# Optimization experiments

Hardware: AMD Instinct MI355X
Metric: run time of the kernel (lower is better)

Reference implementation:

```python
import jax, jax.numpy as jnp
import numpy as np

ENT_N = 100000  # entity vocab (relation rows live inside this table, as in the source)
REL_N = 237
DIM = 128
N = 16384       # batch of triples
EPS = 1e-12     # F.normalize default eps


def _l2norm(x, axis=-1):
    n = jnp.linalg.norm(x, axis=axis, keepdims=True)
    return x / jnp.maximum(n, EPS)


def setup_inputs() -> dict:
    key = jax.random.key(0)
    k1, k2, k3, k4 = jax.random.split(key, 4)
    ent_emb = jax.random.normal(k1, (ENT_N, DIM), dtype=jnp.float32)
    h_ids = jax.random.randint(k2, (N,), 0, ENT_N)
    r_typ = jax.random.randint(k3, (N,), 0, REL_N)
    t_ids = jax.random.randint(k4, (N,), 0, ENT_N)
    return {"ent_emb": ent_emb, "h_ids": h_ids, "r_typ": r_typ, "t_ids": t_ids}


def reference(ent_emb, h_ids, r_typ, t_ids):
    d = ent_emb.shape[1]
    h = _l2norm(ent_emb[h_ids])           # [n, d]
    t = _l2norm(ent_emb[t_ids])           # [n, d]
    # The torch loop looks up ent_emb[r_typ*d + k] for k in range(d); gather
    # the whole relation block at once instead of d tiny lookups + cat.
    r_idx = r_typ[:, None] * d + jnp.arange(d)  # [n, d]
    R = ent_emb[r_idx]                     # [n, d, d]; row k = relation vec k
    prod = jnp.einsum('nd,nkd->nk', h, R)  # [n, d]
    prod = _l2norm(prod)
    return jnp.linalg.norm(prod - t, axis=1)  # [n]
```

## Files before the change

### kernel.cpp

```cpp
#include <hip/hip_runtime.h>

#define RELS 237
#define DIM 128
#define CH 32
#define MAXCHUNK 742
#define EPS 1e-12f

typedef __attribute__((ext_vector_type(8))) short bf16x8;
typedef __attribute__((ext_vector_type(4))) float f32x4;


__device__ __forceinline__ unsigned short f2bf(float f) {
    unsigned int u = __float_as_uint(f);
    u = (u + 0x7fffu + ((u >> 16) & 1u)) >> 16;
    return (unsigned short)u;
}

__global__ void k_count(const int* __restrict__ r_typ, int* __restrict__ ws, int n) {
    int i = blockIdx.x * blockDim.x + threadIdx.x;
    if (i < n) atomicAdd(&ws[r_typ[i]], 1);
}

__global__ void k_scanlist(int* __restrict__ ws) {
    __shared__ int scn[256];
    const int t = threadIdx.x;
    const int c = (t < RELS) ? ws[t] : 0;
    scn[t] = c; __syncthreads();
    #pragma unroll
    for (int off = 1; off < 256; off <<= 1) {
        int v = (t >= off) ? scn[t - off] : 0;
        __syncthreads();
        scn[t] += v; __syncthreads();
    }
    const int base = scn[t] - c;
    if (t < RELS) { ws[320 + t] = base; ws[576 + t] = base; }
    const int nch = (c + CH - 1) >> 5;
    __syncthreads();
    scn[t] = nch; __syncthreads();
    #pragma unroll
    for (int off = 1; off < 256; off <<= 1) {
        int v = (t >= off) ? scn[t - off] : 0;
        __syncthreads();
        scn[t] += v; __syncthreads();
    }
    const int choff = scn[t] - nch;
    if (t == 255) ws[300] = scn[255];
    for (int j = 0; j < nch; ++j) {
        int cb  = base + j * CH;
        int len = c - j * CH; if (len > CH) len = CH;
        ws[1024 + choff + j] = (t << 20) | (cb << 6) | len;
    }
}

__global__ void k_scatter(const int* __restrict__ r_typ, int* __restrict__ ws, int n) {
    int i = blockIdx.x * blockDim.x + threadIdx.x;
    if (i < n) {
        int pos = atomicAdd(&ws[576 + r_typ[i]], 1);
        ws[2048 + pos] = i;
    }
}

__global__ __launch_bounds__(256, 3) void relgemm(
    const float* __restrict__ ent,
    const int*   __restrict__ h_ids,
    const int*   __restrict__ t_ids,
    const int*   __restrict__ ws,
    float*       __restrict__ out)
{
    __shared__ char smem[43648];
    unsigned short* Rb = (unsigned short*)smem;
    unsigned short* Hb = (unsigned short*)(smem + 34816);
    int*  sidx = (int*)(smem + 43520);
    float* Pp  = (float*)smem;

    const int cid = blockIdx.x;
    if (cid >= ws[300]) return;
    const int e    = ws[1024 + cid];
    const int r    = e >> 20;
    const int base = (e >> 6) & 16383;
    const int len  = e & 63;
    const int* sorted = ws + 2048;

    const int tid  = threadIdx.x;
    const int lane = tid & 63;
    const int w    = tid >> 6;

    if (tid < CH) {
        int tc = tid < len ? tid : len - 1;
        sidx[tid] = sorted[base + tc];
    }
    __syncthreads();

    const float4* Rg = (const float4*)ent + ((long)r << 12);
    #pragma unroll
    for (int s = 0; s < 16; ++s) {
        int g = s * 256 + tid;
        int row = g >> 5, c4 = g & 31;
        float4 v = Rg[g];
        ushort4 b; b.x = f2bf(v.x); b.y = f2bf(v.y); b.z = f2bf(v.z); b.w = f2bf(v.w);
        *(ushort4*)(Rb + row * 136 + c4 * 4) = b;
    }
    #pragma unroll
    for (int s = 0; s < 4; ++s) {
        int g = s * 256 + tid;
        int trow = g >> 5, c4 = g & 31;
        int hid = h_ids[sidx[trow]];
        float4 v = ((const float4*)ent)[((long)hid << 5) + c4];
        ushort4 b; b.x = f2bf(v.x); b.y = f2bf(v.y); b.z = f2bf(v.z); b.w = f2bf(v.w);
        *(ushort4*)(Hb + trow * 136 + c4 * 4) = b;
    }
    __syncthreads();

    const int q = lane >> 4, c = lane & 15;
    const unsigned short* A0p = Hb + c * 136 + q * 8;
    const unsigned short* A1p = Hb + (c + 16) * 136 + q * 8;
    const unsigned short* B0p = Rb + (w * 32 + c) * 136 + q * 8;
    const unsigned short* B1p = Rb + (w * 32 + 16 + c) * 136 + q * 8;

    f32x4 a00 = {0.f,0.f,0.f,0.f}, a01 = a00, a10 = a00, a11 = a00;
    #pragma unroll
    for (int ks = 0; ks < 4; ++ks) {
        bf16x8 A0 = *(const bf16x8*)(A0p + ks * 32);
        bf16x8 A1 = *(const bf16x8*)(A1p + ks * 32);
        bf16x8 B0 = *(const bf16x8*)(B0p + ks * 32);
        bf16x8 B1 = *(const bf16x8*)(B1p + ks * 32);
        a00 = __builtin_amdgcn_mfma_f32_16x16x32_bf16(A0, B0, a00, 0, 0, 0);
        a01 = __builtin_amdgcn_mfma_f32_16x16x32_bf16(A0, B1, a01, 0, 0, 0);
        a10 = __builtin_amdgcn_mfma_f32_16x16x32_bf16(A1, B0, a10, 0, 0, 0);
        a11 = __builtin_amdgcn_mfma_f32_16x16x32_bf16(A1, B1, a11, 0, 0, 0);
    }
    __syncthreads();

    #pragma unroll
    for (int reg = 0; reg < 4; ++reg) {
        int m0 = q * 4 + reg;
        Pp[m0 * 132        + w * 32      + c] = a00[reg];
        Pp[m0 * 132        + w * 32 + 16 + c] = a01[reg];
        Pp[(m0 + 16) * 132 + w * 32      + c] = a10[reg];
        Pp[(m0 + 16) * 132 + w * 32 + 16 + c] = a11[reg];
    }
    __syncthreads();

    #pragma unroll
    for (int tt = 0; tt < 8; ++tt) {
        int t   = w * 8 + tt;
        int idx = sidx[t];
        int trow = __builtin_amdgcn_readfirstlane(t_ids[idx]);
        const float* tv = ent + ((long)trow << 7);
        float tv0 = tv[lane], tv1 = tv[lane + 64];
        float p0 = Pp[t * 132 + lane], p1 = Pp[t * 132 + 64 + lane];
        float sp  = p0 * p0 + p1 * p1;
        float st  = tv0 * tv0 + tv1 * tv1;
        float spt = p0 * tv0 + p1 * tv1;
        #pragma unroll
        for (int m = 32; m >= 1; m >>= 1) {
            sp  += __shfl_xor(sp,  m, 64);
            st  += __shfl_xor(st,  m, 64);
            spt += __shfl_xor(spt, m, 64);
        }
        if (lane == 0 && t < len) {
            float npn = fmaxf(sqrtf(sp), EPS);
            float ntn = fmaxf(sqrtf(st), EPS);
            float v   = 2.0f - 2.0f * (spt / (npn * ntn));
            out[idx] = sqrtf(fmaxf(v, 0.0f));
        }
    }
}

extern "C" void kernel_launch(void* const* d_in, const int* in_sizes, int n_in,
                              void* d_out, int out_size, void* d_ws, size_t ws_size,
                              hipStream_t stream) {
    const float* ent   = (const float*)d_in[0];
    const int*   h_ids = (const int*)d_in[1];
    const int*   r_typ = (const int*)d_in[2];
    const int*   t_ids = (const int*)d_in[3];
    float* out = (float*)d_out;
    int*   ws  = (int*)d_ws;
    const int n = in_sizes[1];
    const int nb = (n + 255) / 256;

    hipMemsetAsync(ws, 0, 1024, stream);
    hipLaunchKernelGGL(k_count,    dim3(nb),       dim3(256), 0, stream, r_typ, ws, n);
    hipLaunchKernelGGL(k_scanlist, dim3(1),        dim3(256), 0, stream, ws);
    hipLaunchKernelGGL(k_scatter,  dim3(nb),       dim3(256), 0, stream, r_typ, ws, n);
    hipLaunchKernelGGL(relgemm,    dim3(MAXCHUNK), dim3(256), 0, stream,
                       ent, h_ids, t_ids, ws, out);
}
```

Baseline: 122.9 us.

## Double triple-chunk size per relation block and fuse count with scan

Raises the chunk of triples per block from 32 to 64, so each block's load and bf16 conversion of the 128x128 relation matrix is shared by twice as many triples, and each wave now computes four M-tiles. It also folds the count and scan kernels into one, using a last-block-done atomic counter, which removes one launch. The chunk length is stored as len-1 so a length of 64 fits in the 6-bit field. The costs are more LDS per block, fewer blocks in flight, and more padded waste for relations with few triples.

```diff
diff --git a/kernel.cpp b/kernel.cpp
--- a/kernel.cpp
+++ b/kernel.cpp
@@ -2,8 +2,8 @@
 
 #define RELS 237
 #define DIM 128
-#define CH 32
-#define MAXCHUNK 742
+#define CH 64
+#define MAXCHUNK 489
 #define EPS 1e-12f
 
 typedef __attribute__((ext_vector_type(8))) short bf16x8;
@@ -16,15 +16,18 @@
     return (unsigned short)u;
 }
 
-__global__ void k_count(const int* __restrict__ r_typ, int* __restrict__ ws, int n) {
-    int i = blockIdx.x * blockDim.x + threadIdx.x;
+__global__ void k_count_scan(const int* __restrict__ r_typ, int* __restrict__ ws, int n) {
+    __shared__ int scn[256];
+    __shared__ int amLast;
+    const int t = threadIdx.x;
+    const int i = blockIdx.x * blockDim.x + t;
     if (i < n) atomicAdd(&ws[r_typ[i]], 1);
-}
+    __threadfence();
+    if (t == 0) amLast = (atomicAdd(&ws[255], 1) == (int)gridDim.x - 1);
+    __syncthreads();
+    if (!amLast) return;
 
-__global__ void k_scanlist(int* __restrict__ ws) {
-    __shared__ int scn[256];
-    const int t = threadIdx.x;
-    const int c = (t < RELS) ? ws[t] : 0;
+    const int c = (t < RELS) ? atomicAdd(&ws[t], 0) : 0;
     scn[t] = c; __syncthreads();
     #pragma unroll
     for (int off = 1; off < 256; off <<= 1) {
@@ -34,7 +37,7 @@
     }
     const int base = scn[t] - c;
     if (t < RELS) { ws[320 + t] = base; ws[576 + t] = base; }
-    const int nch = (c + CH - 1) >> 5;
+    const int nch = (c + CH - 1) >> 6;
     __syncthreads();
     scn[t] = nch; __syncthreads();
     #pragma unroll
@@ -48,7 +51,7 @@
     for (int j = 0; j < nch; ++j) {
         int cb  = base + j * CH;
         int len = c - j * CH; if (len > CH) len = CH;
-        ws[1024 + choff + j] = (t << 20) | (cb << 6) | len;
+        ws[1024 + choff + j] = (t << 20) | (cb << 6) | (len - 1);
     }
 }
 
@@ -67,10 +70,10 @@
     const int*   __restrict__ ws,
     float*       __restrict__ out)
 {
-    __shared__ char smem[43648];
+    __shared__ char smem[52480];
     unsigned short* Rb = (unsigned short*)smem;
     unsigned short* Hb = (unsigned short*)(smem + 34816);
-    int*  sidx = (int*)(smem + 43520);
+    int*  sidx = (int*)(smem + 52224);
     float* Pp  = (float*)smem;
 
     const int cid = blockIdx.x;
@@ -78,7 +81,7 @@
     const int e    = ws[1024 + cid];
     const int r    = e >> 20;
     const int base = (e >> 6) & 16383;
-    const int len  = e & 63;
+    const int len  = (e & 63) + 1;
     const int* sorted = ws + 2048;
 
     const int tid  = threadIdx.x;
@@ -101,7 +104,7 @@
         *(ushort4*)(Rb + row * 136 + c4 * 4) = b;
     }
     #pragma unroll
-    for (int s = 0; s < 4; ++s) {
+    for (int s = 0; s < 8; ++s) {
         int g = s * 256 + tid;
         int trow = g >> 5, c4 = g & 31;
         int hid = h_ids[sidx[trow]];
@@ -111,39 +114,44 @@
     }
     __syncthreads();
 
-    const int q = lane >> 4, c = lane & 15;
-    const unsigned short* A0p = Hb + c * 136 + q * 8;
-    const unsigned short* A1p = Hb + (c + 16) * 136 + q * 8;
-    const unsigned short* B0p = Rb + (w * 32 + c) * 136 + q * 8;
-    const unsigned short* B1p = Rb + (w * 32 + 16 + c) * 136 + q * 8;
+    const int q = lane >> 4, cc = lane & 15;
+    const unsigned short* Ap0 = Hb + cc * 136 + q * 8;
+    const unsigned short* Bp0 = Rb + (w * 32 + cc) * 136 + q * 8;
+    const unsigned short* Bp1 = Rb + (w * 32 + 16 + cc) * 136 + q * 8;
 
-    f32x4 a00 = {0.f,0.f,0.f,0.f}, a01 = a00, a10 = a00, a11 = a00;
+    f32x4 acc[4][2];
+    #pragma unroll
+    for (int mt = 0; mt < 4; ++mt)
+        #pragma unroll
+        for (int nt = 0; nt < 2; ++nt)
+            acc[mt][nt] = (f32x4){0.f, 0.f, 0.f, 0.f};
+
     #pragma unroll
     for (int ks = 0; ks < 4; ++ks) {
-        bf16x8 A0 = *(const bf16x8*)(A0p + ks * 32);
-        bf16x8 A1 = *(const bf16x8*)(A1p + ks * 32);
-        bf16x8 B0 = *(const bf16x8*)(B0p + ks * 32);
-        bf16x8 B1 = *(const bf16x8*)(B1p + ks * 32);
-        a00 = __builtin_amdgcn_mfma_f32_16x16x32_bf16(A0, B0, a00, 0, 0, 0);
-        a01 = __builtin_amdgcn_mfma_f32_16x16x32_bf16(A0, B1, a01, 0, 0, 0);
-        a10 = __builtin_amdgcn_mfma_f32_16x16x32_bf16(A1, B0, a10, 0, 0, 0);
-        a11 = __builtin_amdgcn_mfma_f32_16x16x32_bf16(A1, B1, a11, 0, 0, 0);
+        bf16x8 B0 = *(const bf16x8*)(Bp0 + ks * 32);
+        bf16x8 B1 = *(const bf16x8*)(Bp1 + ks * 32);
+        #pragma unroll
+        for (int mt = 0; mt < 4; ++mt) {
+            bf16x8 A = *(const bf16x8*)(Ap0 + mt * 16 * 136 + ks * 32);
+            acc[mt][0] = __builtin_amdgcn_mfma_f32_16x16x32_bf16(A, B0, acc[mt][0], 0, 0, 0);
+            acc[mt][1] = __builtin_amdgcn_mfma_f32_16x16x32_bf16(A, B1, acc[mt][1], 0, 0, 0);
+        }
     }
     __syncthreads();
 
     #pragma unroll
-    for (int reg = 0; reg < 4; ++reg) {
-        int m0 = q * 4 + reg;
-        Pp[m0 * 132        + w * 32      + c] = a00[reg];
-        Pp[m0 * 132        + w * 32 + 16 + c] = a01[reg];
-        Pp[(m0 + 16) * 132 + w * 32      + c] = a10[reg];
-        Pp[(m0 + 16) * 132 + w * 32 + 16 + c] = a11[reg];
-    }
+    for (int mt = 0; mt < 4; ++mt)
+        #pragma unroll
+        for (int reg = 0; reg < 4; ++reg) {
+            int m0 = mt * 16 + q * 4 + reg;
+            Pp[m0 * 132 + w * 32      + cc] = acc[mt][0][reg];
+            Pp[m0 * 132 + w * 32 + 16 + cc] = acc[mt][1][reg];
+        }
     __syncthreads();
 
     #pragma unroll
-    for (int tt = 0; tt < 8; ++tt) {
-        int t   = w * 8 + tt;
+    for (int tt = 0; tt < 16; ++tt) {
+        int t   = w * 16 + tt;
         int idx = sidx[t];
         int trow = __builtin_amdgcn_readfirstlane(t_ids[idx]);
         const float* tv = ent + ((long)trow << 7);
@@ -180,9 +188,8 @@
     const int nb = (n + 255) / 256;
 
     hipMemsetAsync(ws, 0, 1024, stream);
-    hipLaunchKernelGGL(k_count,    dim3(nb),       dim3(256), 0, stream, r_typ, ws, n);
-    hipLaunchKernelGGL(k_scanlist, dim3(1),        dim3(256), 0, stream, ws);
-    hipLaunchKernelGGL(k_scatter,  dim3(nb),       dim3(256), 0, stream, r_typ, ws, n);
-    hipLaunchKernelGGL(relgemm,    dim3(MAXCHUNK), dim3(256), 0, stream,
+    hipLaunchKernelGGL(k_count_scan, dim3(nb),       dim3(256), 0, stream, r_typ, ws, n);
+    hipLaunchKernelGGL(k_scatter,    dim3(nb),       dim3(256), 0, stream, r_typ, ws, n);
+    hipLaunchKernelGGL(relgemm,      dim3(MAXCHUNK), dim3(256), 0, stream,
                        ent, h_ids, t_ids, ws, out);
 }
```

Measured after the change: 129.6 us. +5.5%, slower.
